# Kernel tuning notes

Hardware: AMD Instinct MI355X
Metric: run time of the kernel (lower is better)

Reference implementation:

```python
import jax, jax.numpy as jnp
import numpy as np

N, T, C = 4, 2048, 1024
H = 16
D = C // H  # head_dim = 64


def setup_inputs() -> dict:
    key = jax.random.key(0)
    ks = jax.random.split(key, 6)
    s = 1.0 / np.sqrt(C)
    return {
        "x": jax.random.normal(ks[0], (N, T, C), dtype=jnp.float32),
        "Wq": jax.random.normal(ks[1], (C, C), dtype=jnp.float32) * s,
        "Wk": jax.random.normal(ks[2], (C, C), dtype=jnp.float32) * s,
        "Wv": jax.random.normal(ks[3], (C, C), dtype=jnp.float32) * s,
        "Wo": jax.random.normal(ks[4], (C, C), dtype=jnp.float32) * s,
        "bo": jax.random.normal(ks[5], (C,), dtype=jnp.float32) * s,
    }


def reference(x, Wq, Wk, Wv, Wo, bo):
    n, t, c = x.shape
    # torch nn.Linear: y = x @ W.T
    q = (x @ Wq.T).reshape(n, t, H, D).transpose(0, 2, 1, 3)  # [N,H,T,D]
    k = (x @ Wk.T).reshape(n, t, H, D).transpose(0, 2, 1, 3)
    v = (x @ Wv.T).reshape(n, t, H, D).transpose(0, 2, 1, 3)
    # NOTE: module scales by sqrt(embed_dim), not sqrt(head_dim)
    energy = jnp.einsum("nhqd,nhkd->nhqk", q, k) / jnp.sqrt(jnp.float32(c))
    causal = jnp.tril(jnp.ones((t, t), dtype=bool))  # [T,T]
    energy = jnp.where(causal[None, None], energy, -jnp.inf)
    attn = jax.nn.softmax(energy, axis=-1)
    out = jnp.einsum("nhqk,nhkd->nhqd", attn, v)  # [N,H,T,D]
    out = out.transpose(0, 2, 1, 3).reshape(n, t, c)
    return out @ Wo.T + bo
```

## Files before the change

### kernel.cpp

```cpp
#include <hip/hip_runtime.h>
#include <math.h>

#define N_ 4
#define T_ 2048
#define C_ 1024
#define H_ 16
#define D_ 64
#define NTC (N_*T_*C_)
#define WELEM (C_*C_)

typedef float f32x4  __attribute__((ext_vector_type(4)));
typedef float f32x16 __attribute__((ext_vector_type(16)));
typedef short bf16x8 __attribute__((ext_vector_type(8)));

static __device__ __forceinline__ unsigned short f2bf(float f) {
    union { float f; unsigned u; } v; v.f = f;
    unsigned r = v.u + 0x7FFFu + ((v.u >> 16) & 1u);
    return (unsigned short)(r >> 16);
}

static __device__ __forceinline__ unsigned cvtpk(float lo, float hi) {
    unsigned r;
    asm("v_cvt_pk_bf16_f32 %0, %1, %2" : "=v"(r) : "v"(lo), "v"(hi));
    return r;
}
#define PLSWAP(a, b) asm("v_permlane32_swap_b32 %0, %1" : "+v"(a), "+v"(b))

#define GLDS16(gptr, lptr) \
    __builtin_amdgcn_global_load_lds((const __attribute__((address_space(1))) void*)(gptr), \
                                     (__attribute__((address_space(3))) void*)(lptr), 16, 0, 0)

__global__ __launch_bounds__(256) void cast_x(const float* __restrict__ src,
                                              unsigned short* __restrict__ dst) {
    const int i = blockIdx.x * 256 + threadIdx.x;
    const float4 a = ((const float4*)src)[i * 2];
    const float4 b = ((const float4*)src)[i * 2 + 1];
    unsigned short u[8] = {f2bf(a.x), f2bf(a.y), f2bf(a.z), f2bf(a.w),
                           f2bf(b.x), f2bf(b.y), f2bf(b.z), f2bf(b.w)};
    *(uint4*)&dst[(size_t)i * 8] = *(const uint4*)u;
}

__global__ __launch_bounds__(256) void cast_w4(const float* __restrict__ w0,
                                               const float* __restrict__ w1,
                                               const float* __restrict__ w2,
                                               const float* __restrict__ w3,
                                               unsigned short* __restrict__ dst) {
    const int z = blockIdx.y;
    const float* __restrict__ src = (z == 0) ? w0 : (z == 1) ? w1 : (z == 2) ? w2 : w3;
    unsigned short* __restrict__ d = dst + (size_t)z * WELEM;
    const int i = blockIdx.x * 256 + threadIdx.x;
    const float4 a = ((const float4*)src)[i * 2];
    const float4 b = ((const float4*)src)[i * 2 + 1];
    unsigned short u[8] = {f2bf(a.x), f2bf(a.y), f2bf(a.z), f2bf(a.w),
                           f2bf(b.x), f2bf(b.y), f2bf(b.z), f2bf(b.w)};
    *(uint4*)&d[(size_t)i * 8] = *(const uint4*)u;
}

template <int EPI>
__global__ __launch_bounds__(256) void gemm_bf16(const unsigned short* __restrict__ A,
                                                 const unsigned short* __restrict__ B,
                                                 const float* __restrict__ bo,
                                                 void* __restrict__ outp,
                                                 float oscale) {
    __shared__ __align__(16) unsigned short Abuf[128 * 32];
    __shared__ __align__(16) unsigned short Bbuf[128 * 32];

    const int tid  = threadIdx.x;
    const int lane = tid & 63;
    const int w    = tid >> 6;
    const int lo   = lane & 15;
    const int hi   = lane >> 4;
    const int wm   = w >> 1;
    const int wn   = w & 1;
    const int rowBase = blockIdx.x * 128;
    const int colBase = blockIdx.y * 128;

    f32x4 acc[4][4];
    #pragma unroll
    for (int i = 0; i < 4; ++i)
        #pragma unroll
        for (int j = 0; j < 4; ++j) acc[i][j] = (f32x4)(0.f);

    const int i0 = tid, i1 = tid + 256;
    const int r0 = i0 >> 2, s0 = i0 & 3, g0 = s0 ^ ((r0 >> 1) & 3);
    const int r1 = i1 >> 2, s1 = i1 & 3, g1 = s1 ^ ((r1 >> 1) & 3);

    const unsigned short* gA0 = A + (size_t)(rowBase + r0) * C_ + g0 * 8;
    const unsigned short* gA1 = A + (size_t)(rowBase + r1) * C_ + g1 * 8;
    const unsigned short* gB0 = B + (size_t)(colBase + r0) * C_ + g0 * 8;
    const unsigned short* gB1 = B + (size_t)(colBase + r1) * C_ + g1 * 8;

    for (int k0 = 0; k0 < C_; k0 += 32) {
        GLDS16(gA0 + k0, &Abuf[i0 * 8]);
        GLDS16(gA1 + k0, &Abuf[i1 * 8]);
        GLDS16(gB0 + k0, &Bbuf[i0 * 8]);
        GLDS16(gB1 + k0, &Bbuf[i1 * 8]);
        __syncthreads();

        bf16x8 af[4], bf[4];
        #pragma unroll
        for (int mi = 0; mi < 4; ++mi) {
            const int row = wm * 64 + mi * 16 + lo;
            const int slot = hi ^ ((row >> 1) & 3);
            af[mi] = *(const bf16x8*)&Abuf[row * 32 + slot * 8];
        }
        #pragma unroll
        for (int ni = 0; ni < 4; ++ni) {
            const int row = wn * 64 + ni * 16 + lo;
            const int slot = hi ^ ((row >> 1) & 3);
            bf[ni] = *(const bf16x8*)&Bbuf[row * 32 + slot * 8];
        }
        #pragma unroll
        for (int mi = 0; mi < 4; ++mi)
            #pragma unroll
            for (int ni = 0; ni < 4; ++ni)
                acc[mi][ni] = __builtin_amdgcn_mfma_f32_16x16x32_bf16(af[mi], bf[ni], acc[mi][ni], 0, 0, 0);
        __syncthreads();
    }

    if (EPI == 0) {
        unsigned short* __restrict__ Y = (unsigned short*)outp;
        #pragma unroll
        for (int mi = 0; mi < 4; ++mi) {
            #pragma unroll
            for (int r = 0; r < 4; ++r) {
                const int row = rowBase + wm * 64 + mi * 16 + hi * 4 + r;
                const int nn = row >> 11, tt = row & (T_ - 1);
                #pragma unroll
                for (int ni = 0; ni < 4; ++ni) {
                    const int col = colBase + wn * 64 + ni * 16 + lo;
                    const int hh = col >> 6, dd = col & 63;
                    Y[((size_t)((nn * H_ + hh) * T_ + tt)) * D_ + dd] = f2bf(acc[mi][ni][r] * oscale);
                }
            }
        }
    } else if (EPI == 1) {
        float* __restrict__ out = (float*)outp;
        float bias[4];
        #pragma unroll
        for (int ni = 0; ni < 4; ++ni) bias[ni] = bo[colBase + wn * 64 + ni * 16 + lo];
        #pragma unroll
        for (int mi = 0; mi < 4; ++mi) {
            #pragma unroll
            for (int r = 0; r < 4; ++r) {
                const int row = rowBase + wm * 64 + mi * 16 + hi * 4 + r;
                #pragma unroll
                for (int ni = 0; ni < 4; ++ni) {
                    const int col = colBase + wn * 64 + ni * 16 + lo;
                    out[(size_t)row * C_ + col] = acc[mi][ni][r] + bias[ni];
                }
            }
        }
    } else {
        unsigned short* __restrict__ Y = (unsigned short*)outp;
        #pragma unroll
        for (int mi = 0; mi < 4; ++mi) {
            #pragma unroll
            for (int r = 0; r < 4; ++r) {
                const int row = rowBase + wm * 64 + mi * 16 + hi * 4 + r;
                const int nn = row >> 11, tt = row & (T_ - 1);
                #pragma unroll
                for (int ni = 0; ni < 4; ++ni) {
                    const int col = colBase + wn * 64 + ni * 16 + lo;
                    Y[(size_t)((nn * 16 + (col >> 6)) * 64 + (col & 63)) * T_ + tt] = f2bf(acc[mi][ni][r]);
                }
            }
        }
    }
}

__global__ __launch_bounds__(256, 2) void attn_mfma(const unsigned short* __restrict__ qg,
                                                    const unsigned short* __restrict__ kg,
                                                    const unsigned short* __restrict__ vtg,
                                                    unsigned short* __restrict__ ob) {
    __shared__ __align__(16) unsigned short Kt[2][64 * 64];
    __shared__ __align__(16) unsigned short Vt[2][64 * 64];

    const int tid  = threadIdx.x;
    const int w    = tid >> 6;
    const int lane = tid & 63;
    const int ql   = lane & 31;
    const int h    = lane >> 5;
    const int bid  = blockIdx.x;
    const int qtile = 15 - (bid >> 6);
    const int nh   = bid & 63;
    const int qb   = qtile * 128;
    const size_t base  = (size_t)nh * (T_ * D_);
    const size_t vbase = (size_t)nh * 64 * T_;
    const int qrow0 = qb + w * 32;

    bf16x8 qf[4];
    #pragma unroll
    for (int dsl = 0; dsl < 4; ++dsl)
        qf[dsl] = *(const bf16x8*)(qg + base + (size_t)(qrow0 + ql) * D_ + dsl * 16 + h * 8);

    f32x16 acc0 = (f32x16)(0.f), acc1 = (f32x16)(0.f);
    float mrun = -INFINITY, lrun = 0.f;

    const int mynkt  = (qrow0 >> 6) + 1;
    const int nktmax = (qb >> 6) + 2;
    const int csubdiag = (w & 1) + 1;

    const int i0 = tid, i1 = tid + 256;
    const int kr0 = i0 >> 3, kc0 = ((i0 & 7) ^ (kr0 & 7)) * 8;
    const int kr1 = i1 >> 3, kc1 = ((i1 & 7) ^ (kr1 & 7)) * 8;

    #define STAGE(kt_, buf_)                                                            \
        do {                                                                            \
            const int kb_ = (kt_) * 64;                                                 \
            GLDS16(kg + base + (size_t)(kb_ + kr0) * D_ + kc0, &Kt[buf_][i0 * 8]);      \
            GLDS16(kg + base + (size_t)(kb_ + kr1) * D_ + kc1, &Kt[buf_][i1 * 8]);      \
            GLDS16(vtg + vbase + (size_t)kr0 * T_ + kb_ + kc0, &Vt[buf_][i0 * 8]);      \
            GLDS16(vtg + vbase + (size_t)kr1 * T_ + kb_ + kc1, &Vt[buf_][i1 * 8]);      \
        } while (0)

    STAGE(0, 0);
    __syncthreads();
    int cur = 0;

    for (int kt = 0; kt < nktmax; ++kt) {
        if (kt + 1 < nktmax) STAGE(kt + 1, cur ^ 1);

        if (kt < mynkt) {
            const bool diag = (kt == mynkt - 1);
            const int csub = diag ? csubdiag : 2;
            const unsigned short* Kb = Kt[cur];
            const unsigned short* Vb = Vt[cur];

            f32x16 s0, s1;
            __builtin_amdgcn_s_setprio(1);
            {
                f32x16 z = (f32x16)(0.f);
                #pragma unroll
                for (int dsl = 0; dsl < 4; ++dsl) {
                    const bf16x8 ka = *(const bf16x8*)&Kb[ql * 64 + ((dsl * 2 + h) ^ (ql & 7)) * 8];
                    z = __builtin_amdgcn_mfma_f32_32x32x16_bf16(ka, qf[dsl], z, 0, 0, 0);
                }
                s0 = z;
            }
            if (csub > 1) {
                f32x16 z = (f32x16)(0.f);
                #pragma unroll
                for (int dsl = 0; dsl < 4; ++dsl) {
                    const bf16x8 ka = *(const bf16x8*)&Kb[(32 + ql) * 64 + ((dsl * 2 + h) ^ (ql & 7)) * 8];
                    z = __builtin_amdgcn_mfma_f32_32x32x16_bf16(ka, qf[dsl], z, 0, 0, 0);
                }
                s1 = z;
            }
            __builtin_amdgcn_s_setprio(0);

            if (diag) {
                #pragma unroll
                for (int r = 0; r < 16; ++r) {
                    const int rc = (r & 3) + 8 * (r >> 2) + 4 * h;
                    if (csub == 1) { if (rc > ql) s0[r] = -1e30f; }
                    else           { if (rc > ql) s1[r] = -1e30f; }
                }
            }

            float tm = -1e30f;
            #pragma unroll
            for (int r = 0; r < 16; ++r) tm = fmaxf(tm, s0[r]);
            if (csub > 1) {
                #pragma unroll
                for (int r = 0; r < 16; ++r) tm = fmaxf(tm, s1[r]);
            }
            tm = fmaxf(tm, __shfl_xor(tm, 32));

            if (!__all(tm <= mrun + 8.f)) {
                const float mnew = fmaxf(mrun, tm);
                const float fsc = exp2f(mrun - mnew);
                mrun = mnew;
                lrun *= fsc;
                #pragma unroll
                for (int r = 0; r < 16; ++r) {
                    const float f = __shfl(fsc, (r & 3) + 8 * (r >> 2) + 4 * h);
                    acc0[r] *= f; acc1[r] *= f;
                }
            }

            float psum = 0.f;
            #pragma unroll
            for (int r = 0; r < 16; ++r) { s0[r] = exp2f(s0[r] - mrun); psum += s0[r]; }
            if (csub > 1) {
                #pragma unroll
                for (int r = 0; r < 16; ++r) { s1[r] = exp2f(s1[r] - mrun); psum += s1[r]; }
            }
            psum += __shfl_xor(psum, 32);
            lrun += psum;

            bf16x8 pa[4];
            #pragma unroll
            for (int a = 0; a < 2; ++a) {
                if (a < csub) {
                    #pragma unroll
                    for (int b = 0; b < 2; ++b) {
                        const f32x16& P = a ? s1 : s0;
                        unsigned w0 = cvtpk(P[8 * b + 0], P[8 * b + 1]);
                        unsigned w1 = cvtpk(P[8 * b + 2], P[8 * b + 3]);
                        unsigned w2 = cvtpk(P[8 * b + 4], P[8 * b + 5]);
                        unsigned w3 = cvtpk(P[8 * b + 6], P[8 * b + 7]);
                        PLSWAP(w0, w2);
                        PLSWAP(w1, w3);
                        unsigned wd[4] = {w0, w1, w2, w3};
                        pa[2 * a + b] = *(bf16x8*)wd;
                    }
                }
            }

            __builtin_amdgcn_s_setprio(1);
            #pragma unroll
            for (int ks = 0; ks < 4; ++ks) {
                if (ks < 2 * csub) {
                    const bf16x8 vf0 = *(const bf16x8*)&Vb[ql * 64 + ((ks * 2 + h) ^ (ql & 7)) * 8];
                    const bf16x8 vf1 = *(const bf16x8*)&Vb[(32 + ql) * 64 + ((ks * 2 + h) ^ (ql & 7)) * 8];
                    acc0 = __builtin_amdgcn_mfma_f32_32x32x16_bf16(pa[ks], vf0, acc0, 0, 0, 0);
                    acc1 = __builtin_amdgcn_mfma_f32_32x32x16_bf16(pa[ks], vf1, acc1, 0, 0, 0);
                }
            }
            __builtin_amdgcn_s_setprio(0);
        }
        __syncthreads();
        cur ^= 1;
    }

    const float linv = 1.f / lrun;
    const int nn = nh >> 4, hh = nh & 15;
    #pragma unroll
    for (int r = 0; r < 16; ++r) {
        const int rc = (r & 3) + 8 * (r >> 2) + 4 * h;
        const float li = __shfl(linv, rc);
        const size_t rb = (size_t)(nn * T_ + qrow0 + rc) * C_ + hh * 64;
        ob[rb + ql]      = f2bf(acc0[r] * li);
        ob[rb + 32 + ql] = f2bf(acc1[r] * li);
    }
    #undef STAGE
}

extern "C" void kernel_launch(void* const* d_in, const int* in_sizes, int n_in,
                              void* d_out, int out_size, void* d_ws, size_t ws_size,
                              hipStream_t stream) {
    const float* x  = (const float*)d_in[0];
    const float* Wq = (const float*)d_in[1];
    const float* Wk = (const float*)d_in[2];
    const float* Wv = (const float*)d_in[3];
    const float* Wo = (const float*)d_in[4];
    const float* bo = (const float*)d_in[5];
    float* out = (float*)d_out;

    unsigned short* ws = (unsigned short*)d_ws;
    unsigned short* x_bf  = ws;
    unsigned short* w_bf  = x_bf + (size_t)NTC;
    unsigned short* q_bf  = w_bf + (size_t)4 * WELEM;
    unsigned short* k_bf  = q_bf + (size_t)NTC;
    unsigned short* vt_bf = k_bf + (size_t)NTC;
    unsigned short* a_bf  = vt_bf + (size_t)NTC;

    cast_x<<<NTC / (8 * 256), 256, 0, stream>>>(x, x_bf);
    dim3 gw(WELEM / (8 * 256), 4);
    cast_w4<<<gw, 256, 0, stream>>>(Wq, Wk, Wv, Wo, w_bf);

    dim3 gg(N_ * T_ / 128, C_ / 128);
    gemm_bf16<0><<<gg, 256, 0, stream>>>(x_bf, w_bf + 0 * (size_t)WELEM, nullptr, q_bf, 0.03125f * 1.44269504f);
    gemm_bf16<0><<<gg, 256, 0, stream>>>(x_bf, w_bf + 1 * (size_t)WELEM, nullptr, k_bf, 1.0f);
    gemm_bf16<2><<<gg, 256, 0, stream>>>(x_bf, w_bf + 2 * (size_t)WELEM, nullptr, vt_bf, 1.0f);

    attn_mfma<<<(T_ / 128) * (N_ * H_), 256, 0, stream>>>(q_bf, k_bf, vt_bf, a_bf);

    gemm_bf16<1><<<gg, 256, 0, stream>>>(a_bf, w_bf + 3 * (size_t)WELEM, bo, out, 1.0f);
}
```

Measured before the change: 182.8 us.

## Fuse QKV GEMMs into one launch and pair causal query tiles per block

Merges the three Q/K/V projection GEMM launches into one grid with a z dimension selecting the weight and epilogue. The attention kernel now processes two query tiles per block (tile p and 15-p) so every block does the same causal work, halving the grid to 512 blocks and removing tail imbalance. The max reduction is also rewritten as a pairwise tree. Pairing serializes two tiles per block, which lengthens each block's critical path and lowers the number of concurrent blocks.

Result: slower. 191.5 us (+4.7%).

```diff
diff --git a/kernel.cpp b/kernel.cpp
--- a/kernel.cpp
+++ b/kernel.cpp
@@ -56,70 +56,69 @@
     *(uint4*)&d[(size_t)i * 8] = *(const uint4*)u;
 }
 
-template <int EPI>
-__global__ __launch_bounds__(256) void gemm_bf16(const unsigned short* __restrict__ A,
-                                                 const unsigned short* __restrict__ B,
-                                                 const float* __restrict__ bo,
-                                                 void* __restrict__ outp,
-                                                 float oscale) {
-    __shared__ __align__(16) unsigned short Abuf[128 * 32];
-    __shared__ __align__(16) unsigned short Bbuf[128 * 32];
-
-    const int tid  = threadIdx.x;
-    const int lane = tid & 63;
-    const int w    = tid >> 6;
-    const int lo   = lane & 15;
-    const int hi   = lane >> 4;
-    const int wm   = w >> 1;
-    const int wn   = w & 1;
-    const int rowBase = blockIdx.x * 128;
-    const int colBase = blockIdx.y * 128;
-
-    f32x4 acc[4][4];
-    #pragma unroll
-    for (int i = 0; i < 4; ++i)
-        #pragma unroll
-        for (int j = 0; j < 4; ++j) acc[i][j] = (f32x4)(0.f);
-
-    const int i0 = tid, i1 = tid + 256;
-    const int r0 = i0 >> 2, s0 = i0 & 3, g0 = s0 ^ ((r0 >> 1) & 3);
-    const int r1 = i1 >> 2, s1 = i1 & 3, g1 = s1 ^ ((r1 >> 1) & 3);
-
-    const unsigned short* gA0 = A + (size_t)(rowBase + r0) * C_ + g0 * 8;
-    const unsigned short* gA1 = A + (size_t)(rowBase + r1) * C_ + g1 * 8;
-    const unsigned short* gB0 = B + (size_t)(colBase + r0) * C_ + g0 * 8;
-    const unsigned short* gB1 = B + (size_t)(colBase + r1) * C_ + g1 * 8;
-
-    for (int k0 = 0; k0 < C_; k0 += 32) {
-        GLDS16(gA0 + k0, &Abuf[i0 * 8]);
-        GLDS16(gA1 + k0, &Abuf[i1 * 8]);
-        GLDS16(gB0 + k0, &Bbuf[i0 * 8]);
-        GLDS16(gB1 + k0, &Bbuf[i1 * 8]);
-        __syncthreads();
-
-        bf16x8 af[4], bf[4];
-        #pragma unroll
-        for (int mi = 0; mi < 4; ++mi) {
-            const int row = wm * 64 + mi * 16 + lo;
-            const int slot = hi ^ ((row >> 1) & 3);
-            af[mi] = *(const bf16x8*)&Abuf[row * 32 + slot * 8];
-        }
-        #pragma unroll
-        for (int ni = 0; ni < 4; ++ni) {
-            const int row = wn * 64 + ni * 16 + lo;
-            const int slot = hi ^ ((row >> 1) & 3);
-            bf[ni] = *(const bf16x8*)&Bbuf[row * 32 + slot * 8];
-        }
-        #pragma unroll
-        for (int mi = 0; mi < 4; ++mi)
-            #pragma unroll
-            for (int ni = 0; ni < 4; ++ni)
-                acc[mi][ni] = __builtin_amdgcn_mfma_f32_16x16x32_bf16(af[mi], bf[ni], acc[mi][ni], 0, 0, 0);
-        __syncthreads();
+#define GEMM_BODY(Aptr, Bptr)                                                           \
+    __shared__ __align__(16) unsigned short Abuf[128 * 32];                             \
+    __shared__ __align__(16) unsigned short Bbuf[128 * 32];                             \
+    const int tid  = threadIdx.x;                                                       \
+    const int lane = tid & 63;                                                          \
+    const int w    = tid >> 6;                                                          \
+    const int lo   = lane & 15;                                                         \
+    const int hi   = lane >> 4;                                                         \
+    const int wm   = w >> 1;                                                            \
+    const int wn   = w & 1;                                                             \
+    const int rowBase = blockIdx.x * 128;                                               \
+    const int colBase = blockIdx.y * 128;                                               \
+    f32x4 acc[4][4];                                                                    \
+    _Pragma("unroll")                                                                   \
+    for (int i = 0; i < 4; ++i)                                                         \
+        _Pragma("unroll")                                                               \
+        for (int j = 0; j < 4; ++j) acc[i][j] = (f32x4)(0.f);                           \
+    const int i0 = tid, i1 = tid + 256;                                                 \
+    const int r0 = i0 >> 2, s0_ = i0 & 3, g0 = s0_ ^ ((r0 >> 1) & 3);                   \
+    const int r1 = i1 >> 2, s1_ = i1 & 3, g1 = s1_ ^ ((r1 >> 1) & 3);                   \
+    const unsigned short* gA0 = (Aptr) + (size_t)(rowBase + r0) * C_ + g0 * 8;          \
+    const unsigned short* gA1 = (Aptr) + (size_t)(rowBase + r1) * C_ + g1 * 8;          \
+    const unsigned short* gB0 = (Bptr) + (size_t)(colBase + r0) * C_ + g0 * 8;          \
+    const unsigned short* gB1 = (Bptr) + (size_t)(colBase + r1) * C_ + g1 * 8;          \
+    for (int k0 = 0; k0 < C_; k0 += 32) {                                               \
+        GLDS16(gA0 + k0, &Abuf[i0 * 8]);                                                \
+        GLDS16(gA1 + k0, &Abuf[i1 * 8]);                                                \
+        GLDS16(gB0 + k0, &Bbuf[i0 * 8]);                                                \
+        GLDS16(gB1 + k0, &Bbuf[i1 * 8]);                                                \
+        __syncthreads();                                                                \
+        bf16x8 af[4], bfv[4];                                                           \
+        _Pragma("unroll")                                                               \
+        for (int mi = 0; mi < 4; ++mi) {                                                \
+            const int row = wm * 64 + mi * 16 + lo;                                     \
+            const int slot = hi ^ ((row >> 1) & 3);                                     \
+            af[mi] = *(const bf16x8*)&Abuf[row * 32 + slot * 8];                        \
+        }                                                                               \
+        _Pragma("unroll")                                                               \
+        for (int ni = 0; ni < 4; ++ni) {                                                \
+            const int row = wn * 64 + ni * 16 + lo;                                     \
+            const int slot = hi ^ ((row >> 1) & 3);                                     \
+            bfv[ni] = *(const bf16x8*)&Bbuf[row * 32 + slot * 8];                       \
+        }                                                                               \
+        _Pragma("unroll")                                                               \
+        for (int mi = 0; mi < 4; ++mi)                                                  \
+            _Pragma("unroll")                                                           \
+            for (int ni = 0; ni < 4; ++ni)                                              \
+                acc[mi][ni] = __builtin_amdgcn_mfma_f32_16x16x32_bf16(af[mi], bfv[ni],  \
+                                                                     acc[mi][ni], 0, 0, 0); \
+        __syncthreads();                                                                \
     }
 
-    if (EPI == 0) {
-        unsigned short* __restrict__ Y = (unsigned short*)outp;
+__global__ __launch_bounds__(256) void qkv_fused(const unsigned short* __restrict__ A,
+                                                 const unsigned short* __restrict__ Wall,
+                                                 unsigned short* __restrict__ qkvout) {
+    const int z = blockIdx.z;
+    const unsigned short* __restrict__ B = Wall + (size_t)z * WELEM;
+    unsigned short* __restrict__ Y = qkvout + (size_t)z * NTC;
+    const float oscale = (z == 0) ? (0.03125f * 1.44269504f) : 1.0f;
+
+    GEMM_BODY(A, B)
+
+    if (z < 2) {
         #pragma unroll
         for (int mi = 0; mi < 4; ++mi) {
             #pragma unroll
@@ -129,30 +128,12 @@
                 #pragma unroll
                 for (int ni = 0; ni < 4; ++ni) {
                     const int col = colBase + wn * 64 + ni * 16 + lo;
-                    const int hh = col >> 6, dd = col & 63;
-                    Y[((size_t)((nn * H_ + hh) * T_ + tt)) * D_ + dd] = f2bf(acc[mi][ni][r] * oscale);
-                }
-            }
-        }
-    } else if (EPI == 1) {
-        float* __restrict__ out = (float*)outp;
-        float bias[4];
-        #pragma unroll
-        for (int ni = 0; ni < 4; ++ni) bias[ni] = bo[colBase + wn * 64 + ni * 16 + lo];
-        #pragma unroll
-        for (int mi = 0; mi < 4; ++mi) {
-            #pragma unroll
-            for (int r = 0; r < 4; ++r) {
-                const int row = rowBase + wm * 64 + mi * 16 + hi * 4 + r;
-                #pragma unroll
-                for (int ni = 0; ni < 4; ++ni) {
-                    const int col = colBase + wn * 64 + ni * 16 + lo;
-                    out[(size_t)row * C_ + col] = acc[mi][ni][r] + bias[ni];
+                    Y[((size_t)((nn * H_ + (col >> 6)) * T_ + tt)) * D_ + (col & 63)] =
+                        f2bf(acc[mi][ni][r] * oscale);
                 }
             }
         }
     } else {
-        unsigned short* __restrict__ Y = (unsigned short*)outp;
         #pragma unroll
         for (int mi = 0; mi < 4; ++mi) {
             #pragma unroll
@@ -162,8 +143,32 @@
                 #pragma unroll
                 for (int ni = 0; ni < 4; ++ni) {
                     const int col = colBase + wn * 64 + ni * 16 + lo;
-                    Y[(size_t)((nn * 16 + (col >> 6)) * 64 + (col & 63)) * T_ + tt] = f2bf(acc[mi][ni][r]);
-                }
+                    Y[(size_t)((nn * 16 + (col >> 6)) * 64 + (col & 63)) * T_ + tt] =
+                        f2bf(acc[mi][ni][r]);
+                }
+            }
+        }
+    }
+}
+
+__global__ __launch_bounds__(256) void out_gemm(const unsigned short* __restrict__ A,
+                                                const unsigned short* __restrict__ B,
+                                                const float* __restrict__ bo,
+                                                float* __restrict__ out) {
+    GEMM_BODY(A, B)
+
+    float bias[4];
+    #pragma unroll
+    for (int ni = 0; ni < 4; ++ni) bias[ni] = bo[colBase + wn * 64 + ni * 16 + lo];
+    #pragma unroll
+    for (int mi = 0; mi < 4; ++mi) {
+        #pragma unroll
+        for (int r = 0; r < 4; ++r) {
+            const int row = rowBase + wm * 64 + mi * 16 + hi * 4 + r;
+            #pragma unroll
+            for (int ni = 0; ni < 4; ++ni) {
+                const int col = colBase + wn * 64 + ni * 16 + lo;
+                out[(size_t)row * C_ + col] = acc[mi][ni][r] + bias[ni];
             }
         }
     }
@@ -181,25 +186,16 @@
     const int lane = tid & 63;
     const int ql   = lane & 31;
     const int h    = lane >> 5;
-    const int bid  = blockIdx.x;
-    const int qtile = 15 - (bid >> 6);
-    const int nh   = bid & 63;
-    const int qb   = qtile * 128;
+    const int p    = blockIdx.x >> 6;
+    const int nh   = blockIdx.x & 63;
     const size_t base  = (size_t)nh * (T_ * D_);
     const size_t vbase = (size_t)nh * 64 * T_;
-    const int qrow0 = qb + w * 32;
-
-    bf16x8 qf[4];
-    #pragma unroll
-    for (int dsl = 0; dsl < 4; ++dsl)
-        qf[dsl] = *(const bf16x8*)(qg + base + (size_t)(qrow0 + ql) * D_ + dsl * 16 + h * 8);
-
-    f32x16 acc0 = (f32x16)(0.f), acc1 = (f32x16)(0.f);
-    float mrun = -INFINITY, lrun = 0.f;
-
-    const int mynkt  = (qrow0 >> 6) + 1;
-    const int nktmax = (qb >> 6) + 2;
-    const int csubdiag = (w & 1) + 1;
+    const int nn = nh >> 4, hh = nh & 15;
+
+    const int qt_a = 15 - p, qt_b = p;
+    const int nkt_a = 2 * qt_a + 2;
+    const int nkt_b = 2 * qt_b + 2;
+    const int total = nkt_a + nkt_b;
 
     const int i0 = tid, i1 = tid + 256;
     const int kr0 = i0 >> 3, kc0 = ((i0 & 7) ^ (kr0 & 7)) * 8;
@@ -214,12 +210,52 @@
             GLDS16(vtg + vbase + (size_t)kr1 * T_ + kb_ + kc1, &Vt[buf_][i1 * 8]);      \
         } while (0)
 
+    int qrow0 = qt_a * 128 + w * 32;
+    int mynkt = 2 * qt_a + (w >> 1) + 1;
+    const int csubdiag = (w & 1) + 1;
+
+    bf16x8 qf[4];
+    #pragma unroll
+    for (int dsl = 0; dsl < 4; ++dsl)
+        qf[dsl] = *(const bf16x8*)(qg + base + (size_t)(qrow0 + ql) * D_ + dsl * 16 + h * 8);
+
+    f32x16 acc0 = (f32x16)(0.f), acc1 = (f32x16)(0.f);
+    float mrun = -INFINITY, lrun = 0.f;
+
+    #define EPILOGUE(qr_)                                                               \
+        do {                                                                            \
+            const float linv = 1.f / lrun;                                              \
+            _Pragma("unroll")                                                           \
+            for (int r = 0; r < 16; ++r) {                                              \
+                const int rc = (r & 3) + 8 * (r >> 2) + 4 * h;                          \
+                const float li = __shfl(linv, rc);                                      \
+                const size_t rb = (size_t)(nn * T_ + (qr_) + rc) * C_ + hh * 64;        \
+                ob[rb + ql]      = f2bf(acc0[r] * li);                                  \
+                ob[rb + 32 + ql] = f2bf(acc1[r] * li);                                  \
+            }                                                                           \
+        } while (0)
+
     STAGE(0, 0);
     __syncthreads();
     int cur = 0;
 
-    for (int kt = 0; kt < nktmax; ++kt) {
-        if (kt + 1 < nktmax) STAGE(kt + 1, cur ^ 1);
+    for (int i = 0; i < total; ++i) {
+        const int kt = (i < nkt_a) ? i : i - nkt_a;
+        if (i + 1 < total) {
+            const int ktn = (i + 1 < nkt_a) ? i + 1 : i + 1 - nkt_a;
+            STAGE(ktn, cur ^ 1);
+        }
+
+        if (i == nkt_a) {
+            EPILOGUE(qrow0);
+            qrow0 = qt_b * 128 + w * 32;
+            mynkt = 2 * qt_b + (w >> 1) + 1;
+            #pragma unroll
+            for (int dsl = 0; dsl < 4; ++dsl)
+                qf[dsl] = *(const bf16x8*)(qg + base + (size_t)(qrow0 + ql) * D_ + dsl * 16 + h * 8);
+            acc0 = (f32x16)(0.f); acc1 = (f32x16)(0.f);
+            mrun = -INFINITY; lrun = 0.f;
+        }
 
         if (kt < mynkt) {
             const bool diag = (kt == mynkt - 1);
@@ -258,12 +294,12 @@
                 }
             }
 
-            float tm = -1e30f;
-            #pragma unroll
-            for (int r = 0; r < 16; ++r) tm = fmaxf(tm, s0[r]);
+            float tm = fmaxf(s0[0], s0[1]);
+            #pragma unroll
+            for (int r = 2; r < 16; r += 2) tm = fmaxf(tm, fmaxf(s0[r], s0[r + 1]));
             if (csub > 1) {
                 #pragma unroll
-                for (int r = 0; r < 16; ++r) tm = fmaxf(tm, s1[r]);
+                for (int r = 0; r < 16; r += 2) tm = fmaxf(tm, fmaxf(s1[r], s1[r + 1]));
             }
             tm = fmaxf(tm, __shfl_xor(tm, 32));
 
@@ -324,17 +360,9 @@
         cur ^= 1;
     }
 
-    const float linv = 1.f / lrun;
-    const int nn = nh >> 4, hh = nh & 15;
-    #pragma unroll
-    for (int r = 0; r < 16; ++r) {
-        const int rc = (r & 3) + 8 * (r >> 2) + 4 * h;
-        const float li = __shfl(linv, rc);
-        const size_t rb = (size_t)(nn * T_ + qrow0 + rc) * C_ + hh * 64;
-        ob[rb + ql]      = f2bf(acc0[r] * li);
-        ob[rb + 32 + ql] = f2bf(acc1[r] * li);
-    }
+    EPILOGUE(qrow0);
     #undef STAGE
+    #undef EPILOGUE
 }
 
 extern "C" void kernel_launch(void* const* d_in, const int* in_sizes, int n_in,
@@ -349,23 +377,20 @@
     float* out = (float*)d_out;
 
     unsigned short* ws = (unsigned short*)d_ws;
-    unsigned short* x_bf  = ws;
-    unsigned short* w_bf  = x_bf + (size_t)NTC;
-    unsigned short* q_bf  = w_bf + (size_t)4 * WELEM;
-    unsigned short* k_bf  = q_bf + (size_t)NTC;
-    unsigned short* vt_bf = k_bf + (size_t)NTC;
-    unsigned short* a_bf  = vt_bf + (size_t)NTC;
+    unsigned short* x_bf   = ws;
+    unsigned short* w_bf   = x_bf + (size_t)NTC;
+    unsigned short* qkv_bf = w_bf + (size_t)4 * WELEM;
+    unsigned short* a_bf   = qkv_bf + (size_t)3 * NTC;
 
     cast_x<<<NTC / (8 * 256), 256, 0, stream>>>(x, x_bf);
     dim3 gw(WELEM / (8 * 256), 4);
     cast_w4<<<gw, 256, 0, stream>>>(Wq, Wk, Wv, Wo, w_bf);
 
+    dim3 gq(N_ * T_ / 128, C_ / 128, 3);
+    qkv_fused<<<gq, 256, 0, stream>>>(x_bf, w_bf, qkv_bf);
+
+    attn_mfma<<<512, 256, 0, stream>>>(qkv_bf, qkv_bf + (size_t)NTC, qkv_bf + (size_t)2 * NTC, a_bf);
+
     dim3 gg(N_ * T_ / 128, C_ / 128);
-    gemm_bf16<0><<<gg, 256, 0, stream>>>(x_bf, w_bf + 0 * (size_t)WELEM, nullptr, q_bf, 0.03125f * 1.44269504f);
-    gemm_bf16<0><<<gg, 256, 0, stream>>>(x_bf, w_bf + 1 * (size_t)WELEM, nullptr, k_bf, 1.0f);
-    gemm_bf16<2><<<gg, 256, 0, stream>>>(x_bf, w_bf + 2 * (size_t)WELEM, nullptr, vt_bf, 1.0f);
-
-    attn_mfma<<<(T_ / 128) * (N_ * H_), 256, 0, stream>>>(q_bf, k_bf, vt_bf, a_bf);
-
-    gemm_bf16<1><<<gg, 256, 0, stream>>>(a_bf, w_bf + 3 * (size_t)WELEM, bo, out, 1.0f);
-}
+    out_gemm<<<gg, 256, 0, stream>>>(a_bf, w_bf + 3 * (size_t)WELEM, bo, out);
+}
```
